# Kernel tuning notes

Hardware: AMD Instinct MI355X
Metric: run time of the kernel (lower is better)

The kernel has to match this reference:

```python
import jax, jax.numpy as jnp
import numpy as np

S, B, I, H, L = 256, 64, 512, 512, 2
EPS = 1e-5


def _layer_norm(x, g, b):
    m = jnp.mean(x, axis=-1, keepdims=True)
    v = jnp.var(x, axis=-1, keepdims=True)
    return (x - m) * jax.lax.rsqrt(v + EPS) * g + b


def setup_inputs() -> dict:
    key = jax.random.key(0)
    ks = jax.random.split(key, 8)
    gain = float(np.sqrt(1.0 / H))
    inputs = jax.random.normal(ks[0], (S, B, I), dtype=jnp.float32)
    h0 = jnp.zeros((L, B, H), dtype=jnp.float32)
    c0 = jnp.zeros((L, B, H), dtype=jnp.float32)
    # stacked weights (input_size == hidden_size so wx is uniform across layers)
    wx = jax.random.uniform(ks[1], (L, I, 4 * H), minval=-gain, maxval=gain, dtype=jnp.float32)
    wh = jax.random.uniform(ks[2], (L, H, 4 * H), minval=-gain, maxval=gain, dtype=jnp.float32)
    bias = jax.random.uniform(ks[3], (L, 4 * H), minval=-gain, maxval=gain, dtype=jnp.float32)
    # LayerNorm affine params: norm[2l] applied to x@wx, norm[2l+1] applied to h@wh
    ln_gx = jnp.ones((L, 4 * H), dtype=jnp.float32)
    ln_bx = jnp.zeros((L, 4 * H), dtype=jnp.float32)
    ln_gh = jnp.ones((L, 4 * H), dtype=jnp.float32)
    ln_bh = jnp.zeros((L, 4 * H), dtype=jnp.float32)
    return {"inputs": inputs, "h0": h0, "c0": c0, "wx": wx, "wh": wh,
            "bias": bias, "ln_gx": ln_gx, "ln_bx": ln_bx, "ln_gh": ln_gh, "ln_bh": ln_bh}


def reference(inputs, h0, c0, wx, wh, bias, ln_gx, ln_bx, ln_gh, ln_bh):
    x = inputs  # [S, B, I]
    hs, cs = [], []
    for l in range(L):
        # input-to-gate projection + its LayerNorm is time-independent: precompute
        xw = jnp.einsum('sbi,io->sbo', x, wx[l])            # [S, B, 4H]
        xn = _layer_norm(xw, ln_gx[l], ln_bx[l]) + bias[l]  # [S, B, 4H]
        whl, gh, bh = wh[l], ln_gh[l], ln_bh[l]

        def step(carry, xt):
            h, c = carry
            gate = xt + _layer_norm(h @ whl, gh, bh)        # [B, 4H]
            i, f, o, u = jnp.split(gate, 4, axis=-1)
            c = jax.nn.sigmoid(f) * c + jax.nn.sigmoid(i) * jnp.tanh(u)
            h = jax.nn.sigmoid(o) * jnp.tanh(c)
            return (h, c), h

        (hN, cN), ys = jax.lax.scan(step, (h0[l], c0[l]), xn)
        hs.append(hN)
        cs.append(cN)
        x = ys  # [S, B, H]
    h_n = jnp.stack(hs, axis=0)  # [L, B, H]
    c_n = jnp.stack(cs, axis=0)
    return x, h_n, c_n
```

## Files before the change

### kernel.cpp

```cpp
#include <hip/hip_runtime.h>

typedef unsigned short u16;
typedef _Float16 f16;
typedef __attribute__((ext_vector_type(8))) _Float16 f16x8;
typedef __attribute__((ext_vector_type(8))) unsigned short u16x8;
typedef __attribute__((ext_vector_type(4))) float f32x4;
typedef __attribute__((ext_vector_type(4))) unsigned u32x4;

#define NWG 32

__device__ __forceinline__ unsigned split2(float v) {
  f16 h = (f16)v;
  f16 l2 = (f16)((v - (float)h) * 2048.0f);
  return (unsigned)__builtin_bit_cast(u16, h) | ((unsigned)__builtin_bit_cast(u16, l2) << 16);
}

__global__ void k_zero(unsigned* __restrict__ part, unsigned* __restrict__ flg) {
  int i = blockIdx.x * blockDim.x + threadIdx.x;
  if (i < 8192) { part[i] = 0u; flg[i] = 0u; }
}

__global__ void k_wsplit(const float* __restrict__ wx, u16* __restrict__ th, u16* __restrict__ tl) {
  __shared__ float tile[32][33];
  int l = blockIdx.z;
  int n0 = blockIdx.x * 32, k0 = blockIdx.y * 32;
  int tx = threadIdx.x, ty = threadIdx.y;
  const float* src = wx + (size_t)l * 512 * 2048;
#pragma unroll
  for (int i = 0; i < 4; ++i)
    tile[ty + i * 8][tx] = src[(size_t)(k0 + ty + i * 8) * 2048 + n0 + tx];
  __syncthreads();
  u16* dh = th + (size_t)l * 2048 * 512;
  u16* dl = tl + (size_t)l * 2048 * 512;
#pragma unroll
  for (int i = 0; i < 4; ++i) {
    unsigned s = split2(tile[tx][ty + i * 8]);
    dh[(size_t)(n0 + ty + i * 8) * 512 + k0 + tx] = (u16)s;
    dl[(size_t)(n0 + ty + i * 8) * 512 + k0 + tx] = (u16)(s >> 16);
  }
}

__global__ void k_wlo(const float* __restrict__ wh, u16* __restrict__ wlo) {
  int idx = blockIdx.x * blockDim.x + threadIdx.x;
  int l = idx >> 17;
  int r = idx & 131071;
  int lane = r & 63;
  int fg = r >> 6;
  int kc = fg & 15, q = (fg >> 4) & 3, g = fg >> 6;
  int gcol = g * 16 + (lane & 15) + q * 512;
  int kb = kc * 32 + ((lane >> 4) << 3);
  const float* W = wh + (size_t)l * 512 * 2048;
  u16x8 o;
#pragma unroll
  for (int j = 0; j < 8; ++j)
    o[j] = (u16)(split2(W[(size_t)(kb + j) * 2048 + gcol]) >> 16);
  *(u16x8*)(wlo + (size_t)idx * 8) = o;
}

__global__ void __launch_bounds__(256, 1) k_gemm3(const float* __restrict__ A,
                                                  const u16* __restrict__ Bh, const u16* __restrict__ Bl,
                                                  float* __restrict__ C, int N, int K) {
  __shared__ u16 sA[2][128 * 64];
  __shared__ u16 sB[2][128 * 64];
  const int tid = threadIdx.x, l = tid & 63, w = tid >> 6;
  const int bx = blockIdx.x, by = blockIdx.y;
  const int wr = (w >> 1) * 64, wc = (w & 1) * 64;
  f32x4 acc0[4][4] = {}, acc1[4][4] = {};
  for (int k0 = 0; k0 < K; k0 += 64) {
#pragma unroll
    for (int s = 0; s < 4; ++s) {
      int cn = s * 256 + tid;
      int row = cn >> 3;
      int f0 = (cn & 7) * 8;
      int kb = f0 * 2;
      int sw = row * 128 + (kb ^ ((row & 7) << 4));
      const float* ap = A + ((size_t)(by * 128 + row) * K + k0 + f0);
      float4 a0 = *(const float4*)ap, a1 = *(const float4*)(ap + 4);
      float av[8] = {a0.x, a0.y, a0.z, a0.w, a1.x, a1.y, a1.z, a1.w};
      u16x8 ah_, al_;
#pragma unroll
      for (int j = 0; j < 8; ++j) {
        unsigned sp = split2(av[j]);
        ah_[j] = (u16)sp;
        al_[j] = (u16)(sp >> 16);
      }
      *(u16x8*)((char*)sA[0] + sw) = ah_;
      *(u16x8*)((char*)sA[1] + sw) = al_;
      size_t gb = (((size_t)(bx * 128 + row) * K + k0) << 1) + kb;
      *(u16x8*)((char*)sB[0] + sw) = *(const u16x8*)((const char*)Bh + gb);
      *(u16x8*)((char*)sB[1] + sw) = *(const u16x8*)((const char*)Bl + gb);
    }
    __syncthreads();
#pragma unroll
    for (int kc = 0; kc < 2; ++kc) {
      int kb = kc * 64 + (l >> 4) * 16;
      f16x8 ah[4], al[4], bh[4], bl[4];
#pragma unroll
      for (int mt = 0; mt < 4; ++mt) {
        int row = wr + mt * 16 + (l & 15);
        int off = row * 128 + (kb ^ ((row & 7) << 4));
        ah[mt] = *(const f16x8*)((const char*)sA[0] + off);
        al[mt] = *(const f16x8*)((const char*)sA[1] + off);
      }
#pragma unroll
      for (int nt = 0; nt < 4; ++nt) {
        int col = wc + nt * 16 + (l & 15);
        int off = col * 128 + (kb ^ ((col & 7) << 4));
        bh[nt] = *(const f16x8*)((const char*)sB[0] + off);
        bl[nt] = *(const f16x8*)((const char*)sB[1] + off);
      }
#pragma unroll
      for (int mt = 0; mt < 4; ++mt)
#pragma unroll
        for (int nt = 0; nt < 4; ++nt) {
          acc0[mt][nt] = __builtin_amdgcn_mfma_f32_16x16x32_f16(ah[mt], bh[nt], acc0[mt][nt], 0, 0, 0);
          acc1[mt][nt] = __builtin_amdgcn_mfma_f32_16x16x32_f16(ah[mt], bl[nt], acc1[mt][nt], 0, 0, 0);
          acc1[mt][nt] = __builtin_amdgcn_mfma_f32_16x16x32_f16(al[mt], bh[nt], acc1[mt][nt], 0, 0, 0);
        }
    }
    __syncthreads();
  }
#pragma unroll
  for (int mt = 0; mt < 4; ++mt)
#pragma unroll
    for (int nt = 0; nt < 4; ++nt)
#pragma unroll
      for (int j = 0; j < 4; ++j) {
        int row = by * 128 + wr + mt * 16 + ((l >> 4) << 2) + j;
        int col = bx * 128 + wc + nt * 16 + (l & 15);
        C[(size_t)row * N + col] = acc0[mt][nt][j] + acc1[mt][nt][j] * (1.0f / 2048.0f);
      }
}

__global__ void __launch_bounds__(256) k_ln2(float* __restrict__ X, const float* __restrict__ g,
                                             const float* __restrict__ b, const float* __restrict__ bias) {
  const int row = blockIdx.x, tid = threadIdx.x;
  float* rp = X + (size_t)row * 2048 + tid * 8;
  float4 v0 = *(const float4*)rp, v1 = *(const float4*)(rp + 4);
  float x[8] = {v0.x, v0.y, v0.z, v0.w, v1.x, v1.y, v1.z, v1.w};
  float s1 = 0.f, s2 = 0.f;
#pragma unroll
  for (int j = 0; j < 8; ++j) { s1 += x[j]; s2 += x[j] * x[j]; }
#pragma unroll
  for (int m = 1; m <= 32; m <<= 1) { s1 += __shfl_xor(s1, m, 64); s2 += __shfl_xor(s2, m, 64); }
  __shared__ float a1[4], a2[4];
  if ((tid & 63) == 0) { a1[tid >> 6] = s1; a2[tid >> 6] = s2; }
  __syncthreads();
  s1 = a1[0] + a1[1] + a1[2] + a1[3];
  s2 = a2[0] + a2[1] + a2[2] + a2[3];
  float mu = s1 * (1.f / 2048.f);
  float var = s2 * (1.f / 2048.f) - mu * mu;
  float rstd = 1.0f / sqrtf(var + 1e-5f);
#pragma unroll
  for (int j = 0; j < 8; ++j) {
    int c = tid * 8 + j;
    x[j] = (x[j] - mu) * rstd * g[c] + b[c] + bias[c];
  }
  *(float4*)rp = {x[0], x[1], x[2], x[3]};
  *(float4*)(rp + 4) = {x[4], x[5], x[6], x[7]};
}

__global__ void __launch_bounds__(256, 1) k_scan6(
    const float* __restrict__ wh, const u16* __restrict__ wlo,
    const float* __restrict__ gh, const float* __restrict__ bh,
    const float* __restrict__ xn, const float* __restrict__ h0l, const float* __restrict__ c0l,
    unsigned* __restrict__ hpubp, float* __restrict__ cspill,
    unsigned long long* __restrict__ part, unsigned* __restrict__ flags,
    float* __restrict__ ys, float* __restrict__ hn, float* __restrict__ cn,
    int t0, int first) {
  __shared__ u16 pk[32768];
  __shared__ u16 wl[32768];
  __shared__ float musd[128];
  const int tid = threadIdx.x;
  const int l = tid & 63, w = tid >> 6;
  const int g = blockIdx.x;
  const int lq = l >> 4, ll = l & 15;
  const int hcol = g * 16 + ll;

  const u16* wloG = wlo + (size_t)g * 32768;
  for (int c = tid; c < 4096; c += 256) {
    int lane = c & 63, kc = (c >> 6) & 15, q = c >> 10;
    int gcol = g * 16 + (lane & 15) + q * 512;
    int kb = kc * 32 + ((lane >> 4) << 3);
    u16x8 t8;
#pragma unroll
    for (int j = 0; j < 8; ++j)
      t8[j] = __builtin_bit_cast(u16, (f16)wh[(size_t)(kb + j) * 2048 + gcol]);
    *(u16x8*)(pk + (size_t)c * 8) = t8;
    *(u16x8*)(wl + (size_t)c * 8) = *(const u16x8*)(wloG + (size_t)c * 8);
  }
  float gam[4], bet[4];
#pragma unroll
  for (int q = 0; q < 4; ++q) { int gc = hcol + q * 512; gam[q] = gh[gc]; bet[q] = bh[gc]; }
  float cr[4];
#pragma unroll
  for (int j = 0; j < 4; ++j) {
    int r = w * 16 + lq * 4 + j;
    cr[j] = first ? c0l[r * 512 + hcol] : cspill[r * 512 + hcol];
  }
  if (first) {
    for (int u = tid; u < 1024; u += 256) {
      int row = 2 * g + (u >> 9), col = u & 511;
      __hip_atomic_store(&hpubp[row * 512 + col], split2(h0l[row * 512 + col]),
                         __ATOMIC_RELAXED, __HIP_MEMORY_SCOPE_AGENT);
    }
  }
  unsigned bid = 0;
#define BAR_ARRIVE()                                                                         \
  do {                                                                                       \
    bid++;                                                                                   \
    asm volatile("s_waitcnt vmcnt(0)" ::: "memory");                                         \
    __syncthreads();                                                                         \
    if (tid == 0)                                                                            \
      __hip_atomic_store(&flags[g * 32], bid, __ATOMIC_RELAXED, __HIP_MEMORY_SCOPE_AGENT);   \
  } while (0)
#define BAR_WAIT()                                                                           \
  do {                                                                                       \
    if (tid < NWG)                                                                           \
      while (__hip_atomic_load(&flags[tid * 32], __ATOMIC_RELAXED,                           \
                               __HIP_MEMORY_SCOPE_AGENT) < bid) {}                           \
    __builtin_amdgcn_fence(__ATOMIC_ACQUIRE, "agent");                                       \
  } while (0)

  float xp[16];
  BAR_ARRIVE();
#pragma unroll
  for (int q = 0; q < 4; ++q)
#pragma unroll
    for (int j = 0; j < 4; ++j)
      xp[q * 4 + j] = xn[(size_t)(w * 16 + lq * 4 + j) * 2048 + hcol + q * 512];
  BAR_WAIT();
  __syncthreads();

  for (int t = 0; t < 128; ++t) {
    const int p = (t0 + t) & 1;
    f32x4 acc0[4] = {}, acc1[4] = {};
#pragma unroll
    for (int kc = 0; kc < 16; ++kc) {
      const unsigned* hp = hpubp + ((size_t)(w * 16 + ll) * 512 + kc * 32 + lq * 8);
      uint4 pa = *(const uint4*)hp;
      uint4 pb = *(const uint4*)(hp + 4);
      u32x4 ahw, alw;
      ahw[0] = __builtin_amdgcn_perm(pa.y, pa.x, 0x05040100u);
      ahw[1] = __builtin_amdgcn_perm(pa.w, pa.z, 0x05040100u);
      ahw[2] = __builtin_amdgcn_perm(pb.y, pb.x, 0x05040100u);
      ahw[3] = __builtin_amdgcn_perm(pb.w, pb.z, 0x05040100u);
      alw[0] = __builtin_amdgcn_perm(pa.y, pa.x, 0x07060302u);
      alw[1] = __builtin_amdgcn_perm(pa.w, pa.z, 0x07060302u);
      alw[2] = __builtin_amdgcn_perm(pb.y, pb.x, 0x07060302u);
      alw[3] = __builtin_amdgcn_perm(pb.w, pb.z, 0x07060302u);
      f16x8 ah = __builtin_bit_cast(f16x8, ahw);
      f16x8 al = __builtin_bit_cast(f16x8, alw);
#pragma unroll
      for (int q = 0; q < 4; ++q) {
        f16x8 bhv = *(const f16x8*)(pk + ((size_t)(q * 16 + kc) * 64 + l) * 8);
        f16x8 blv = *(const f16x8*)(wl + ((size_t)(q * 16 + kc) * 64 + l) * 8);
        acc0[q] = __builtin_amdgcn_mfma_f32_16x16x32_f16(ah, bhv, acc0[q], 0, 0, 0);
        acc1[q] = __builtin_amdgcn_mfma_f32_16x16x32_f16(ah, blv, acc1[q], 0, 0, 0);
        acc1[q] = __builtin_amdgcn_mfma_f32_16x16x32_f16(al, bhv, acc1[q], 0, 0, 0);
      }
    }
    float y[4][4];
#pragma unroll
    for (int q = 0; q < 4; ++q)
#pragma unroll
      for (int j = 0; j < 4; ++j)
        y[q][j] = acc0[q][j] + acc1[q][j] * (1.0f / 2048.0f);

    float s1[4], s2[4];
#pragma unroll
    for (int j = 0; j < 4; ++j) {
      s1[j] = y[0][j] + y[1][j] + y[2][j] + y[3][j];
      s2[j] = y[0][j] * y[0][j] + y[1][j] * y[1][j] + y[2][j] * y[2][j] + y[3][j] * y[3][j];
    }
#pragma unroll
    for (int m = 1; m <= 8; m <<= 1)
#pragma unroll
      for (int j = 0; j < 4; ++j) {
        s1[j] += __shfl_xor(s1[j], m, 64);
        s2[j] += __shfl_xor(s2[j], m, 64);
      }
    if (ll == 0) {
#pragma unroll
      for (int j = 0; j < 4; ++j) {
        int r = w * 16 + lq * 4 + j;
        unsigned long long pv = ((unsigned long long)__builtin_bit_cast(unsigned, s2[j]) << 32) |
                                (unsigned long long)__builtin_bit_cast(unsigned, s1[j]);
        __hip_atomic_store(&part[(size_t)p * 2048 + (size_t)r * 32 + g], pv,
                           __ATOMIC_RELAXED, __HIP_MEMORY_SCOPE_AGENT);
      }
    }
    BAR_ARRIVE();
    BAR_WAIT();
    if (tid < 64) {
      const uint4* pp = (const uint4*)(part + (size_t)p * 2048 + (size_t)tid * 32);
      float a1 = 0.f, a2 = 0.f;
#pragma unroll
      for (int i = 0; i < 16; ++i) {
        uint4 v = pp[i];
        a1 += __builtin_bit_cast(float, v.x);
        a2 += __builtin_bit_cast(float, v.y);
        a1 += __builtin_bit_cast(float, v.z);
        a2 += __builtin_bit_cast(float, v.w);
      }
      float mu = a1 * (1.f / 2048.f);
      float ex2 = a2 * (1.f / 2048.f);
      musd[tid] = mu;
      musd[64 + tid] = 1.0f / sqrtf(ex2 - mu * mu + 1e-5f);
    }
    __syncthreads();
    float hs[4];
#pragma unroll
    for (int j = 0; j < 4; ++j) {
      int r = w * 16 + lq * 4 + j;
      float mu = musd[r], rstd = musd[64 + r];
      float gv[4];
#pragma unroll
      for (int q = 0; q < 4; ++q)
        gv[q] = (y[q][j] - mu) * rstd * gam[q] + bet[q] + xp[q * 4 + j];
      float fi = 1.f / (1.f + expf(-gv[0]));
      float ff = 1.f / (1.f + expf(-gv[1]));
      float fo = 1.f / (1.f + expf(-gv[2]));
      float fu = tanhf(gv[3]);
      cr[j] = ff * cr[j] + fi * fu;
      float h = fo * tanhf(cr[j]);
      hs[j] = h;
      __hip_atomic_store(&hpubp[(size_t)r * 512 + hcol], split2(h),
                         __ATOMIC_RELAXED, __HIP_MEMORY_SCOPE_AGENT);
    }
    BAR_ARRIVE();
#pragma unroll
    for (int j = 0; j < 4; ++j) {
      int r = w * 16 + lq * 4 + j;
      size_t ro = (size_t)r * 512 + hcol;
      __hip_atomic_store(&ys[(size_t)t * 32768 + ro], hs[j], __ATOMIC_RELAXED, __HIP_MEMORY_SCOPE_AGENT);
      if (t == 127)
        __hip_atomic_store(&cspill[ro], cr[j], __ATOMIC_RELAXED, __HIP_MEMORY_SCOPE_AGENT);
      if (t0 + t == 255) {
        __hip_atomic_store(&hn[ro], hs[j], __ATOMIC_RELAXED, __HIP_MEMORY_SCOPE_AGENT);
        __hip_atomic_store(&cn[ro], cr[j], __ATOMIC_RELAXED, __HIP_MEMORY_SCOPE_AGENT);
      }
    }
    if (t < 127) {
      const float* xrow = xn + (size_t)(t + 1) * 64 * 2048;
#pragma unroll
      for (int q = 0; q < 4; ++q)
#pragma unroll
        for (int j = 0; j < 4; ++j)
          xp[q * 4 + j] = xrow[(size_t)(w * 16 + lq * 4 + j) * 2048 + hcol + q * 512];
    }
    BAR_WAIT();
    __syncthreads();
  }
#undef BAR_ARRIVE
#undef BAR_WAIT
}

#define XN_OFF   0ull
#define WXH_OFF  67108864ull
#define WXL_OFF  71303168ull
#define WLO_OFF  75497472ull
#define HPP_OFF  79691776ull
#define CSP_OFF  79822848ull
#define PART_OFF 79953920ull
#define FLG_OFF  79986688ull

extern "C" void kernel_launch(void* const* d_in, const int* in_sizes, int n_in,
                              void* d_out, int out_size, void* d_ws, size_t ws_size,
                              hipStream_t stream) {
  const float* inputs = (const float*)d_in[0];
  const float* h0 = (const float*)d_in[1];
  const float* c0 = (const float*)d_in[2];
  const float* wx = (const float*)d_in[3];
  const float* wh = (const float*)d_in[4];
  const float* bias = (const float*)d_in[5];
  const float* gx = (const float*)d_in[6];
  const float* bxp = (const float*)d_in[7];
  const float* ghp = (const float*)d_in[8];
  const float* bhp = (const float*)d_in[9];
  float* out = (float*)d_out;
  char* ws = (char*)d_ws;

  float* xn = (float*)(ws + XN_OFF);
  u16* wxh = (u16*)(ws + WXH_OFF);
  u16* wxl = (u16*)(ws + WXL_OFF);
  u16* wlo = (u16*)(ws + WLO_OFF);
  unsigned* hpp = (unsigned*)(ws + HPP_OFF);
  float* csp = (float*)(ws + CSP_OFF);
  unsigned long long* part = (unsigned long long*)(ws + PART_OFF);
  unsigned* flg = (unsigned*)(ws + FLG_OFF);

  k_zero<<<32, 256, 0, stream>>>((unsigned*)(ws + PART_OFF), flg);
  k_wsplit<<<dim3(64, 16, 2), dim3(32, 8), 0, stream>>>(wx, wxh, wxl);
  k_wlo<<<1024, 256, 0, stream>>>(wh, wlo);

  for (int l = 0; l < 2; ++l) {
    const float* Abase = (l == 0) ? inputs : out;
    for (int k = 0; k < 2; ++k) {
      k_gemm3<<<dim3(16, 64), 256, 0, stream>>>(Abase + (size_t)k * 8192 * 512,
                                                wxh + (size_t)l * 2048 * 512,
                                                wxl + (size_t)l * 2048 * 512, xn, 2048, 512);
      k_ln2<<<8192, 256, 0, stream>>>(xn, gx + l * 2048, bxp + l * 2048, bias + l * 2048);
      k_scan6<<<NWG, 256, 0, stream>>>(wh + (size_t)l * 1048576, wlo + (size_t)l * 1048576,
                                       ghp + l * 2048, bhp + l * 2048, xn,
                                       h0 + (size_t)l * 32768, c0 + (size_t)l * 32768,
                                       hpp, csp, part, flg + (size_t)(l * 2 + k) * 2048,
                                       out + (size_t)k * 128 * 32768,
                                       out + 8388608 + (size_t)l * 32768,
                                       out + 8388608 + 65536 + (size_t)l * 32768,
                                       k * 128, (k == 0) ? 1 : 0);
    }
  }
}
```

Baseline: 7.080 ms.

## Run both LSTM layers concurrently in one wavefront-pipelined persistent scan kernel

Layer 1 no longer waits for all of layer 0. A single 64-workgroup persistent kernel runs layer 0 on half the workgroups and layer 1, one step behind, on the other half. Layer 1 computes its input projection and LayerNorm on the fly from layer 0's double-buffered published h. This drops the second input GEMM, the second LayerNorm pass and two scan launches. Weights are now pre-packed into MFMA fragment layout once, but layer 1 reads its low-part weight fragments from global memory each step, and cross-layer flag waits add synchronisation cost.

```diff
diff --git a/kernel.cpp b/kernel.cpp
--- a/kernel.cpp
+++ b/kernel.cpp
@@ -7,54 +7,51 @@
 typedef __attribute__((ext_vector_type(4))) float f32x4;
 typedef __attribute__((ext_vector_type(4))) unsigned u32x4;
 
-#define NWG 32
-
 __device__ __forceinline__ unsigned split2(float v) {
   f16 h = (f16)v;
   f16 l2 = (f16)((v - (float)h) * 2048.0f);
   return (unsigned)__builtin_bit_cast(u16, h) | ((unsigned)__builtin_bit_cast(u16, l2) << 16);
 }
 
-__global__ void k_zero(unsigned* __restrict__ part, unsigned* __restrict__ flg) {
+__device__ __forceinline__ unsigned fld(const unsigned* p) {
+  return __hip_atomic_load(p, __ATOMIC_RELAXED, __HIP_MEMORY_SCOPE_AGENT);
+}
+
+__global__ void k_zero(unsigned* __restrict__ z) {
   int i = blockIdx.x * blockDim.x + threadIdx.x;
-  if (i < 8192) { part[i] = 0u; flg[i] = 0u; }
+  if (i < 32768) z[i] = 0u;
 }
 
 __global__ void k_wsplit(const float* __restrict__ wx, u16* __restrict__ th, u16* __restrict__ tl) {
   __shared__ float tile[32][33];
-  int l = blockIdx.z;
   int n0 = blockIdx.x * 32, k0 = blockIdx.y * 32;
   int tx = threadIdx.x, ty = threadIdx.y;
-  const float* src = wx + (size_t)l * 512 * 2048;
 #pragma unroll
   for (int i = 0; i < 4; ++i)
-    tile[ty + i * 8][tx] = src[(size_t)(k0 + ty + i * 8) * 2048 + n0 + tx];
+    tile[ty + i * 8][tx] = wx[(size_t)(k0 + ty + i * 8) * 2048 + n0 + tx];
   __syncthreads();
-  u16* dh = th + (size_t)l * 2048 * 512;
-  u16* dl = tl + (size_t)l * 2048 * 512;
 #pragma unroll
   for (int i = 0; i < 4; ++i) {
     unsigned s = split2(tile[tx][ty + i * 8]);
-    dh[(size_t)(n0 + ty + i * 8) * 512 + k0 + tx] = (u16)s;
-    dl[(size_t)(n0 + ty + i * 8) * 512 + k0 + tx] = (u16)(s >> 16);
-  }
-}
-
-__global__ void k_wlo(const float* __restrict__ wh, u16* __restrict__ wlo) {
+    th[(size_t)(n0 + ty + i * 8) * 512 + k0 + tx] = (u16)s;
+    tl[(size_t)(n0 + ty + i * 8) * 512 + k0 + tx] = (u16)(s >> 16);
+  }
+}
+
+__global__ void k_pack(const float* __restrict__ W, u16* __restrict__ hi, u16* __restrict__ lo) {
   int idx = blockIdx.x * blockDim.x + threadIdx.x;
-  int l = idx >> 17;
-  int r = idx & 131071;
-  int lane = r & 63;
-  int fg = r >> 6;
-  int kc = fg & 15, q = (fg >> 4) & 3, g = fg >> 6;
+  int lane = idx & 63, kc = (idx >> 6) & 15, q = (idx >> 10) & 3, g = idx >> 12;
   int gcol = g * 16 + (lane & 15) + q * 512;
   int kb = kc * 32 + ((lane >> 4) << 3);
-  const float* W = wh + (size_t)l * 512 * 2048;
-  u16x8 o;
-#pragma unroll
-  for (int j = 0; j < 8; ++j)
-    o[j] = (u16)(split2(W[(size_t)(kb + j) * 2048 + gcol]) >> 16);
-  *(u16x8*)(wlo + (size_t)idx * 8) = o;
+  u16x8 oh, ol;
+#pragma unroll
+  for (int j = 0; j < 8; ++j) {
+    unsigned s = split2(W[(size_t)(kb + j) * 2048 + gcol]);
+    oh[j] = (u16)s;
+    ol[j] = (u16)(s >> 16);
+  }
+  *(u16x8*)(hi + (size_t)idx * 8) = oh;
+  *(u16x8*)(lo + (size_t)idx * 8) = ol;
 }
 
 __global__ void __launch_bounds__(256, 1) k_gemm3(const float* __restrict__ A,
@@ -160,48 +157,71 @@
   *(float4*)(rp + 4) = {x[4], x[5], x[6], x[7]};
 }
 
-__global__ void __launch_bounds__(256, 1) k_scan6(
-    const float* __restrict__ wh, const u16* __restrict__ wlo,
+__device__ __forceinline__ void unpk(uint4 a, uint4 b, f16x8& hi, f16x8& lo) {
+  u32x4 H, L;
+  H[0] = __builtin_amdgcn_perm(a.y, a.x, 0x05040100u);
+  H[1] = __builtin_amdgcn_perm(a.w, a.z, 0x05040100u);
+  H[2] = __builtin_amdgcn_perm(b.y, b.x, 0x05040100u);
+  H[3] = __builtin_amdgcn_perm(b.w, b.z, 0x05040100u);
+  L[0] = __builtin_amdgcn_perm(a.y, a.x, 0x07060302u);
+  L[1] = __builtin_amdgcn_perm(a.w, a.z, 0x07060302u);
+  L[2] = __builtin_amdgcn_perm(b.y, b.x, 0x07060302u);
+  L[3] = __builtin_amdgcn_perm(b.w, b.z, 0x07060302u);
+  hi = __builtin_bit_cast(f16x8, H);
+  lo = __builtin_bit_cast(f16x8, L);
+}
+
+__global__ void __launch_bounds__(256, 1) k_scan9(
+    const float* __restrict__ xn, const u16* __restrict__ frg,
+    const float* __restrict__ gx, const float* __restrict__ bx,
     const float* __restrict__ gh, const float* __restrict__ bh,
-    const float* __restrict__ xn, const float* __restrict__ h0l, const float* __restrict__ c0l,
-    unsigned* __restrict__ hpubp, float* __restrict__ cspill,
-    unsigned long long* __restrict__ part, unsigned* __restrict__ flags,
-    float* __restrict__ ys, float* __restrict__ hn, float* __restrict__ cn,
-    int t0, int first) {
+    const float* __restrict__ bias,
+    const float* __restrict__ h0, const float* __restrict__ c0,
+    unsigned* __restrict__ hp0, unsigned* __restrict__ hp1,
+    unsigned long long* __restrict__ pt0, unsigned long long* __restrict__ pt1,
+    unsigned* __restrict__ f0, unsigned* __restrict__ f1,
+    float* __restrict__ cs0, float* __restrict__ cs1,
+    float* __restrict__ out, int t0, int first) {
   __shared__ u16 pk[32768];
-  __shared__ u16 wl[32768];
-  __shared__ float musd[128];
+  __shared__ u16 sb[32768];
+  __shared__ float musd[256];
   const int tid = threadIdx.x;
   const int l = tid & 63, w = tid >> 6;
   const int g = blockIdx.x;
+  const int layer = g >> 5, gg = g & 31;
   const int lq = l >> 4, ll = l & 15;
-  const int hcol = g * 16 + ll;
-
-  const u16* wloG = wlo + (size_t)g * 32768;
+  const int hcol = gg * 16 + ll;
+  const bool L0 = (layer == 0);
+  unsigned* fown = L0 ? f0 : f1;
+  unsigned* foth = L0 ? f1 : f0;
+
+  const u16* pkG = frg + (size_t)(L0 ? 0 : 2) * 1048576 + (size_t)gg * 32768;
+  const u16* sbG = frg + (size_t)(L0 ? 1 : 4) * 1048576 + (size_t)gg * 32768;
+  const u16* whlG = frg + (size_t)3 * 1048576 + (size_t)gg * 32768;
+  const u16* wxlG = frg + (size_t)5 * 1048576 + (size_t)gg * 32768;
   for (int c = tid; c < 4096; c += 256) {
-    int lane = c & 63, kc = (c >> 6) & 15, q = c >> 10;
-    int gcol = g * 16 + (lane & 15) + q * 512;
-    int kb = kc * 32 + ((lane >> 4) << 3);
-    u16x8 t8;
-#pragma unroll
-    for (int j = 0; j < 8; ++j)
-      t8[j] = __builtin_bit_cast(u16, (f16)wh[(size_t)(kb + j) * 2048 + gcol]);
-    *(u16x8*)(pk + (size_t)c * 8) = t8;
-    *(u16x8*)(wl + (size_t)c * 8) = *(const u16x8*)(wloG + (size_t)c * 8);
-  }
-  float gam[4], bet[4];
-#pragma unroll
-  for (int q = 0; q < 4; ++q) { int gc = hcol + q * 512; gam[q] = gh[gc]; bet[q] = bh[gc]; }
+    *(u16x8*)(pk + (size_t)c * 8) = *(const u16x8*)(pkG + (size_t)c * 8);
+    *(u16x8*)(sb + (size_t)c * 8) = *(const u16x8*)(sbG + (size_t)c * 8);
+  }
+  float gxv[4], bxv[4], ghv[4], bhv[4], biv[4];
+#pragma unroll
+  for (int q = 0; q < 4; ++q) {
+    int gc = layer * 2048 + hcol + q * 512;
+    gxv[q] = gx[gc]; bxv[q] = bx[gc]; ghv[q] = gh[gc]; bhv[q] = bh[gc]; biv[q] = bias[gc];
+  }
   float cr[4];
-#pragma unroll
-  for (int j = 0; j < 4; ++j) {
-    int r = w * 16 + lq * 4 + j;
-    cr[j] = first ? c0l[r * 512 + hcol] : cspill[r * 512 + hcol];
+  {
+    const float* cl = first ? (c0 + (size_t)layer * 32768) : (L0 ? cs0 : cs1);
+#pragma unroll
+    for (int j = 0; j < 4; ++j)
+      cr[j] = cl[(w * 16 + lq * 4 + j) * 512 + hcol];
   }
   if (first) {
+    unsigned* dst = L0 ? (hp0 + 32768) : hp1;
     for (int u = tid; u < 1024; u += 256) {
-      int row = 2 * g + (u >> 9), col = u & 511;
-      __hip_atomic_store(&hpubp[row * 512 + col], split2(h0l[row * 512 + col]),
+      int row = 2 * gg + (u >> 9), col = u & 511;
+      __hip_atomic_store(&dst[row * 512 + col],
+                         split2(h0[(size_t)layer * 32768 + row * 512 + col]),
                          __ATOMIC_RELAXED, __HIP_MEMORY_SCOPE_AGENT);
     }
   }
@@ -212,158 +232,247 @@
     asm volatile("s_waitcnt vmcnt(0)" ::: "memory");                                         \
     __syncthreads();                                                                         \
     if (tid == 0)                                                                            \
-      __hip_atomic_store(&flags[g * 32], bid, __ATOMIC_RELAXED, __HIP_MEMORY_SCOPE_AGENT);   \
+      __hip_atomic_store(&fown[gg * 32], bid, __ATOMIC_RELAXED, __HIP_MEMORY_SCOPE_AGENT);   \
   } while (0)
-#define BAR_WAIT()                                                                           \
+#define BAR_WAIT(XEN, XTHR)                                                                  \
   do {                                                                                       \
-    if (tid < NWG)                                                                           \
-      while (__hip_atomic_load(&flags[tid * 32], __ATOMIC_RELAXED,                           \
-                               __HIP_MEMORY_SCOPE_AGENT) < bid) {}                           \
+    if (tid < 32) {                                                                          \
+      while (fld(&fown[tid * 32]) < bid) {}                                                  \
+    } else if (tid < 64 && (XEN)) {                                                          \
+      unsigned xt_ = (XTHR);                                                                 \
+      while (fld(&foth[(tid - 32) * 32]) < xt_) {}                                           \
+    }                                                                                        \
     __builtin_amdgcn_fence(__ATOMIC_ACQUIRE, "agent");                                       \
   } while (0)
 
   float xp[16];
   BAR_ARRIVE();
-#pragma unroll
-  for (int q = 0; q < 4; ++q)
-#pragma unroll
-    for (int j = 0; j < 4; ++j)
-      xp[q * 4 + j] = xn[(size_t)(w * 16 + lq * 4 + j) * 2048 + hcol + q * 512];
-  BAR_WAIT();
+  if (L0) {
+#pragma unroll
+    for (int q = 0; q < 4; ++q)
+#pragma unroll
+      for (int j = 0; j < 4; ++j)
+        xp[q * 4 + j] = xn[(size_t)(w * 16 + lq * 4 + j) * 2048 + hcol + q * 512];
+  }
+  BAR_WAIT(false, 0u);
   __syncthreads();
 
-  for (int t = 0; t < 128; ++t) {
-    const int p = (t0 + t) & 1;
-    f32x4 acc0[4] = {}, acc1[4] = {};
-#pragma unroll
-    for (int kc = 0; kc < 16; ++kc) {
-      const unsigned* hp = hpubp + ((size_t)(w * 16 + ll) * 512 + kc * 32 + lq * 8);
-      uint4 pa = *(const uint4*)hp;
-      uint4 pb = *(const uint4*)(hp + 4);
-      u32x4 ahw, alw;
-      ahw[0] = __builtin_amdgcn_perm(pa.y, pa.x, 0x05040100u);
-      ahw[1] = __builtin_amdgcn_perm(pa.w, pa.z, 0x05040100u);
-      ahw[2] = __builtin_amdgcn_perm(pb.y, pb.x, 0x05040100u);
-      ahw[3] = __builtin_amdgcn_perm(pb.w, pb.z, 0x05040100u);
-      alw[0] = __builtin_amdgcn_perm(pa.y, pa.x, 0x07060302u);
-      alw[1] = __builtin_amdgcn_perm(pa.w, pa.z, 0x07060302u);
-      alw[2] = __builtin_amdgcn_perm(pb.y, pb.x, 0x07060302u);
-      alw[3] = __builtin_amdgcn_perm(pb.w, pb.z, 0x07060302u);
-      f16x8 ah = __builtin_bit_cast(f16x8, ahw);
-      f16x8 al = __builtin_bit_cast(f16x8, alw);
-#pragma unroll
-      for (int q = 0; q < 4; ++q) {
-        f16x8 bhv = *(const f16x8*)(pk + ((size_t)(q * 16 + kc) * 64 + l) * 8);
-        f16x8 blv = *(const f16x8*)(wl + ((size_t)(q * 16 + kc) * 64 + l) * 8);
-        acc0[q] = __builtin_amdgcn_mfma_f32_16x16x32_f16(ah, bhv, acc0[q], 0, 0, 0);
-        acc1[q] = __builtin_amdgcn_mfma_f32_16x16x32_f16(ah, blv, acc1[q], 0, 0, 0);
-        acc1[q] = __builtin_amdgcn_mfma_f32_16x16x32_f16(al, bhv, acc1[q], 0, 0, 0);
-      }
-    }
-    float y[4][4];
-#pragma unroll
-    for (int q = 0; q < 4; ++q)
-#pragma unroll
-      for (int j = 0; j < 4; ++j)
-        y[q][j] = acc0[q][j] + acc1[q][j] * (1.0f / 2048.0f);
-
-    float s1[4], s2[4];
-#pragma unroll
-    for (int j = 0; j < 4; ++j) {
-      s1[j] = y[0][j] + y[1][j] + y[2][j] + y[3][j];
-      s2[j] = y[0][j] * y[0][j] + y[1][j] * y[1][j] + y[2][j] * y[2][j] + y[3][j] * y[3][j];
-    }
-#pragma unroll
-    for (int m = 1; m <= 8; m <<= 1)
+  for (int r = 0; r < 129; ++r) {
+    const bool act = L0 ? (r < 128) : (r >= 1);
+    const int tl = L0 ? r : r - 1;
+    const int t_abs = t0 + tl;
+    const int p = t_abs & 1;
+    float yx[4][4], yh[4][4];
+    if (act) {
+      if (L0) {
+        const unsigned* hb = hp0 + (size_t)(p ^ 1) * 32768;
+        f32x4 a0[4] = {}, a1[4] = {};
+#pragma unroll
+        for (int kc = 0; kc < 16; ++kc) {
+          const unsigned* hpx = hb + ((size_t)(w * 16 + ll) * 512 + kc * 32 + lq * 8);
+          f16x8 ah, al;
+          unpk(*(const uint4*)hpx, *(const uint4*)(hpx + 4), ah, al);
+#pragma unroll
+          for (int q = 0; q < 4; ++q) {
+            size_t fo = ((size_t)(q * 16 + kc) * 64 + l) * 8;
+            f16x8 bhv_ = *(const f16x8*)(pk + fo);
+            f16x8 blv_ = *(const f16x8*)(sb + fo);
+            a0[q] = __builtin_amdgcn_mfma_f32_16x16x32_f16(ah, bhv_, a0[q], 0, 0, 0);
+            a1[q] = __builtin_amdgcn_mfma_f32_16x16x32_f16(ah, blv_, a1[q], 0, 0, 0);
+            a1[q] = __builtin_amdgcn_mfma_f32_16x16x32_f16(al, bhv_, a1[q], 0, 0, 0);
+          }
+        }
+#pragma unroll
+        for (int q = 0; q < 4; ++q)
+#pragma unroll
+          for (int j = 0; j < 4; ++j)
+            yh[q][j] = a0[q][j] + a1[q][j] * (1.0f / 2048.0f);
+      } else {
+        const unsigned* xb = hp0 + (size_t)p * 32768;
+        f32x4 ax0[4] = {}, ax1[4] = {}, ah0[4] = {}, ah1[4] = {};
+#pragma unroll
+        for (int kc = 0; kc < 16; ++kc) {
+          size_t aoff = (size_t)(w * 16 + ll) * 512 + kc * 32 + lq * 8;
+          f16x8 xah, xal, hah, hal;
+          unpk(*(const uint4*)(xb + aoff), *(const uint4*)(xb + aoff + 4), xah, xal);
+          unpk(*(const uint4*)(hp1 + aoff), *(const uint4*)(hp1 + aoff + 4), hah, hal);
+#pragma unroll
+          for (int q = 0; q < 4; ++q) {
+            size_t fo = ((size_t)(q * 16 + kc) * 64 + l) * 8;
+            f16x8 whh_ = *(const f16x8*)(pk + fo);
+            f16x8 wxh_ = *(const f16x8*)(sb + fo);
+            f16x8 whl_ = *(const f16x8*)(whlG + fo);
+            f16x8 wxl_ = *(const f16x8*)(wxlG + fo);
+            ax0[q] = __builtin_amdgcn_mfma_f32_16x16x32_f16(xah, wxh_, ax0[q], 0, 0, 0);
+            ax1[q] = __builtin_amdgcn_mfma_f32_16x16x32_f16(xah, wxl_, ax1[q], 0, 0, 0);
+            ax1[q] = __builtin_amdgcn_mfma_f32_16x16x32_f16(xal, wxh_, ax1[q], 0, 0, 0);
+            ah0[q] = __builtin_amdgcn_mfma_f32_16x16x32_f16(hah, whh_, ah0[q], 0, 0, 0);
+            ah1[q] = __builtin_amdgcn_mfma_f32_16x16x32_f16(hah, whl_, ah1[q], 0, 0, 0);
+            ah1[q] = __builtin_amdgcn_mfma_f32_16x16x32_f16(hal, whh_, ah1[q], 0, 0, 0);
+          }
+        }
+#pragma unroll
+        for (int q = 0; q < 4; ++q)
+#pragma unroll
+          for (int j = 0; j < 4; ++j) {
+            yx[q][j] = ax0[q][j] + ax1[q][j] * (1.0f / 2048.0f);
+            yh[q][j] = ah0[q][j] + ah1[q][j] * (1.0f / 2048.0f);
+          }
+      }
+      float s1h[4], s2h[4], s1x[4], s2x[4];
 #pragma unroll
       for (int j = 0; j < 4; ++j) {
-        s1[j] += __shfl_xor(s1[j], m, 64);
-        s2[j] += __shfl_xor(s2[j], m, 64);
-      }
-    if (ll == 0) {
+        s1h[j] = yh[0][j] + yh[1][j] + yh[2][j] + yh[3][j];
+        s2h[j] = yh[0][j] * yh[0][j] + yh[1][j] * yh[1][j] + yh[2][j] * yh[2][j] + yh[3][j] * yh[3][j];
+        if (!L0) {
+          s1x[j] = yx[0][j] + yx[1][j] + yx[2][j] + yx[3][j];
+          s2x[j] = yx[0][j] * yx[0][j] + yx[1][j] * yx[1][j] + yx[2][j] * yx[2][j] + yx[3][j] * yx[3][j];
+        }
+      }
+#pragma unroll
+      for (int m = 1; m <= 8; m <<= 1)
+#pragma unroll
+        for (int j = 0; j < 4; ++j) {
+          s1h[j] += __shfl_xor(s1h[j], m, 64);
+          s2h[j] += __shfl_xor(s2h[j], m, 64);
+          if (!L0) {
+            s1x[j] += __shfl_xor(s1x[j], m, 64);
+            s2x[j] += __shfl_xor(s2x[j], m, 64);
+          }
+        }
+      if (ll == 0) {
+#pragma unroll
+        for (int j = 0; j < 4; ++j) {
+          int rr = w * 16 + lq * 4 + j;
+          unsigned long long vh = ((unsigned long long)__builtin_bit_cast(unsigned, s2h[j]) << 32) |
+                                  (unsigned long long)__builtin_bit_cast(unsigned, s1h[j]);
+          if (L0) {
+            __hip_atomic_store(&pt0[(size_t)p * 2048 + (size_t)rr * 32 + gg], vh,
+                               __ATOMIC_RELAXED, __HIP_MEMORY_SCOPE_AGENT);
+          } else {
+            unsigned long long vx = ((unsigned long long)__builtin_bit_cast(unsigned, s2x[j]) << 32) |
+                                    (unsigned long long)__builtin_bit_cast(unsigned, s1x[j]);
+            __hip_atomic_store(&pt1[((size_t)(p * 2 + 0) * 64 + rr) * 32 + gg], vx,
+                               __ATOMIC_RELAXED, __HIP_MEMORY_SCOPE_AGENT);
+            __hip_atomic_store(&pt1[((size_t)(p * 2 + 1) * 64 + rr) * 32 + gg], vh,
+                               __ATOMIC_RELAXED, __HIP_MEMORY_SCOPE_AGENT);
+          }
+        }
+      }
+    }
+    BAR_ARRIVE();
+    BAR_WAIT(L0 && r >= 2, bid - 2);
+    float hs[4];
+    if (act) {
+      if (tid < 64) {
+        if (L0) {
+          const uint4* pp = (const uint4*)(pt0 + (size_t)p * 2048 + (size_t)tid * 32);
+          float a1 = 0.f, a2 = 0.f;
+#pragma unroll
+          for (int i = 0; i < 16; ++i) {
+            uint4 v = pp[i];
+            a1 += __builtin_bit_cast(float, v.x); a2 += __builtin_bit_cast(float, v.y);
+            a1 += __builtin_bit_cast(float, v.z); a2 += __builtin_bit_cast(float, v.w);
+          }
+          float mu = a1 * (1.f / 2048.f), ex2 = a2 * (1.f / 2048.f);
+          musd[tid] = mu;
+          musd[64 + tid] = 1.0f / sqrtf(ex2 - mu * mu + 1e-5f);
+        } else {
+          const uint4* px = (const uint4*)(pt1 + ((size_t)(p * 2 + 0) * 64 + tid) * 32);
+          const uint4* ph = (const uint4*)(pt1 + ((size_t)(p * 2 + 1) * 64 + tid) * 32);
+          float a1x = 0.f, a2x = 0.f, a1h = 0.f, a2h = 0.f;
+#pragma unroll
+          for (int i = 0; i < 16; ++i) {
+            uint4 vx = px[i], vh = ph[i];
+            a1x += __builtin_bit_cast(float, vx.x); a2x += __builtin_bit_cast(float, vx.y);
+            a1x += __builtin_bit_cast(float, vx.z); a2x += __builtin_bit_cast(float, vx.w);
+            a1h += __builtin_bit_cast(float, vh.x); a2h += __builtin_bit_cast(float, vh.y);
+            a1h += __builtin_bit_cast(float, vh.z); a2h += __builtin_bit_cast(float, vh.w);
+          }
+          float mux = a1x * (1.f / 2048.f), ex2x = a2x * (1.f / 2048.f);
+          float muh = a1h * (1.f / 2048.f), ex2h = a2h * (1.f / 2048.f);
+          musd[tid] = mux;
+          musd[64 + tid] = 1.0f / sqrtf(ex2x - mux * mux + 1e-5f);
+          musd[128 + tid] = muh;
+          musd[192 + tid] = 1.0f / sqrtf(ex2h - muh * muh + 1e-5f);
+        }
+      }
+      __syncthreads();
 #pragma unroll
       for (int j = 0; j < 4; ++j) {
-        int r = w * 16 + lq * 4 + j;
-        unsigned long long pv = ((unsigned long long)__builtin_bit_cast(unsigned, s2[j]) << 32) |
-                                (unsigned long long)__builtin_bit_cast(unsigned, s1[j]);
-        __hip_atomic_store(&part[(size_t)p * 2048 + (size_t)r * 32 + g], pv,
-                           __ATOMIC_RELAXED, __HIP_MEMORY_SCOPE_AGENT);
+        int rr = w * 16 + lq * 4 + j;
+        float gv[4];
+        if (L0) {
+          float mu = musd[rr], rstd = musd[64 + rr];
+#pragma unroll
+          for (int q = 0; q < 4; ++q)
+            gv[q] = (yh[q][j] - mu) * rstd * ghv[q] + bhv[q] + xp[q * 4 + j];
+        } else {
+          float mux = musd[rr], rsx = musd[64 + rr];
+          float muh = musd[128 + rr], rsh = musd[192 + rr];
+#pragma unroll
+          for (int q = 0; q < 4; ++q)
+            gv[q] = (yx[q][j] - mux) * rsx * gxv[q] + bxv[q] + biv[q] +
+                    (yh[q][j] - muh) * rsh * ghv[q] + bhv[q];
+        }
+        float fi = 1.f / (1.f + expf(-gv[0]));
+        float ff = 1.f / (1.f + expf(-gv[1]));
+        float fo = 1.f / (1.f + expf(-gv[2]));
+        float fu = tanhf(gv[3]);
+        cr[j] = ff * cr[j] + fi * fu;
+        float h = fo * tanhf(cr[j]);
+        hs[j] = h;
+        size_t ro = (size_t)rr * 512 + hcol;
+        unsigned* dst = L0 ? (hp0 + (size_t)p * 32768) : hp1;
+        __hip_atomic_store(&dst[ro], split2(h), __ATOMIC_RELAXED, __HIP_MEMORY_SCOPE_AGENT);
       }
     }
     BAR_ARRIVE();
-    BAR_WAIT();
-    if (tid < 64) {
-      const uint4* pp = (const uint4*)(part + (size_t)p * 2048 + (size_t)tid * 32);
-      float a1 = 0.f, a2 = 0.f;
-#pragma unroll
-      for (int i = 0; i < 16; ++i) {
-        uint4 v = pp[i];
-        a1 += __builtin_bit_cast(float, v.x);
-        a2 += __builtin_bit_cast(float, v.y);
-        a1 += __builtin_bit_cast(float, v.z);
-        a2 += __builtin_bit_cast(float, v.w);
-      }
-      float mu = a1 * (1.f / 2048.f);
-      float ex2 = a2 * (1.f / 2048.f);
-      musd[tid] = mu;
-      musd[64 + tid] = 1.0f / sqrtf(ex2 - mu * mu + 1e-5f);
-    }
-    __syncthreads();
-    float hs[4];
-#pragma unroll
-    for (int j = 0; j < 4; ++j) {
-      int r = w * 16 + lq * 4 + j;
-      float mu = musd[r], rstd = musd[64 + r];
-      float gv[4];
-#pragma unroll
-      for (int q = 0; q < 4; ++q)
-        gv[q] = (y[q][j] - mu) * rstd * gam[q] + bet[q] + xp[q * 4 + j];
-      float fi = 1.f / (1.f + expf(-gv[0]));
-      float ff = 1.f / (1.f + expf(-gv[1]));
-      float fo = 1.f / (1.f + expf(-gv[2]));
-      float fu = tanhf(gv[3]);
-      cr[j] = ff * cr[j] + fi * fu;
-      float h = fo * tanhf(cr[j]);
-      hs[j] = h;
-      __hip_atomic_store(&hpubp[(size_t)r * 512 + hcol], split2(h),
-                         __ATOMIC_RELAXED, __HIP_MEMORY_SCOPE_AGENT);
-    }
-    BAR_ARRIVE();
-#pragma unroll
-    for (int j = 0; j < 4; ++j) {
-      int r = w * 16 + lq * 4 + j;
-      size_t ro = (size_t)r * 512 + hcol;
-      __hip_atomic_store(&ys[(size_t)t * 32768 + ro], hs[j], __ATOMIC_RELAXED, __HIP_MEMORY_SCOPE_AGENT);
-      if (t == 127)
-        __hip_atomic_store(&cspill[ro], cr[j], __ATOMIC_RELAXED, __HIP_MEMORY_SCOPE_AGENT);
-      if (t0 + t == 255) {
-        __hip_atomic_store(&hn[ro], hs[j], __ATOMIC_RELAXED, __HIP_MEMORY_SCOPE_AGENT);
-        __hip_atomic_store(&cn[ro], cr[j], __ATOMIC_RELAXED, __HIP_MEMORY_SCOPE_AGENT);
-      }
-    }
-    if (t < 127) {
-      const float* xrow = xn + (size_t)(t + 1) * 64 * 2048;
+    if (act) {
+#pragma unroll
+      for (int j = 0; j < 4; ++j) {
+        int rr = w * 16 + lq * 4 + j;
+        size_t ro = (size_t)rr * 512 + hcol;
+        if (!L0)
+          __hip_atomic_store(&out[(size_t)t_abs * 32768 + ro], hs[j],
+                             __ATOMIC_RELAXED, __HIP_MEMORY_SCOPE_AGENT);
+        if (tl == 127)
+          __hip_atomic_store(&(L0 ? cs0 : cs1)[ro], cr[j],
+                             __ATOMIC_RELAXED, __HIP_MEMORY_SCOPE_AGENT);
+        if (t_abs == 255) {
+          __hip_atomic_store(&out[8388608 + (size_t)layer * 32768 + ro], hs[j],
+                             __ATOMIC_RELAXED, __HIP_MEMORY_SCOPE_AGENT);
+          __hip_atomic_store(&out[8388608 + 65536 + (size_t)layer * 32768 + ro], cr[j],
+                             __ATOMIC_RELAXED, __HIP_MEMORY_SCOPE_AGENT);
+        }
+      }
+    }
+    if (L0 && r < 127) {
+      const float* xrow = xn + (size_t)(r + 1) * 64 * 2048;
 #pragma unroll
       for (int q = 0; q < 4; ++q)
 #pragma unroll
         for (int j = 0; j < 4; ++j)
           xp[q * 4 + j] = xrow[(size_t)(w * 16 + lq * 4 + j) * 2048 + hcol + q * 512];
     }
-    BAR_WAIT();
+    BAR_WAIT(!L0, bid);
     __syncthreads();
   }
 #undef BAR_ARRIVE
 #undef BAR_WAIT
 }
 
-#define XN_OFF   0ull
-#define WXH_OFF  67108864ull
-#define WXL_OFF  71303168ull
-#define WLO_OFF  75497472ull
-#define HPP_OFF  79691776ull
-#define CSP_OFF  79822848ull
-#define PART_OFF 79953920ull
-#define FLG_OFF  79986688ull
+#define XN_OFF  0ull
+#define WXH_OFF 67108864ull
+#define WXL_OFF 69206016ull
+#define FRG_OFF 71303168ull
+#define HP0_OFF 83886080ull
+#define HP1_OFF 84148224ull
+#define CS0_OFF 84279296ull
+#define CS1_OFF 84410368ull
+#define PT0_OFF 84541440ull
+#define PT1_OFF 84574208ull
+#define FLG_OFF 84639744ull
 
 extern "C" void kernel_launch(void* const* d_in, const int* in_sizes, int n_in,
                               void* d_out, int out_size, void* d_ws, size_t ws_size,
@@ -374,7 +483,7 @@
   const float* wx = (const float*)d_in[3];
   const float* wh = (const float*)d_in[4];
   const float* bias = (const float*)d_in[5];
-  const float* gx = (const float*)d_in[6];
+  const float* gxp = (const float*)d_in[6];
   const float* bxp = (const float*)d_in[7];
   const float* ghp = (const float*)d_in[8];
   const float* bhp = (const float*)d_in[9];
@@ -384,31 +493,29 @@
   float* xn = (float*)(ws + XN_OFF);
   u16* wxh = (u16*)(ws + WXH_OFF);
   u16* wxl = (u16*)(ws + WXL_OFF);
-  u16* wlo = (u16*)(ws + WLO_OFF);
-  unsigned* hpp = (unsigned*)(ws + HPP_OFF);
-  float* csp = (float*)(ws + CSP_OFF);
-  unsigned long long* part = (unsigned long long*)(ws + PART_OFF);
+  u16* frg = (u16*)(ws + FRG_OFF);
+  unsigned* hp0 = (unsigned*)(ws + HP0_OFF);
+  unsigned* hp1 = (unsigned*)(ws + HP1_OFF);
+  float* cs0 = (float*)(ws + CS0_OFF);
+  float* cs1 = (float*)(ws + CS1_OFF);
+  unsigned long long* pt0 = (unsigned long long*)(ws + PT0_OFF);
+  unsigned long long* pt1 = (unsigned long long*)(ws + PT1_OFF);
   unsigned* flg = (unsigned*)(ws + FLG_OFF);
 
-  k_zero<<<32, 256, 0, stream>>>((unsigned*)(ws + PART_OFF), flg);
-  k_wsplit<<<dim3(64, 16, 2), dim3(32, 8), 0, stream>>>(wx, wxh, wxl);
-  k_wlo<<<1024, 256, 0, stream>>>(wh, wlo);
-
-  for (int l = 0; l < 2; ++l) {
-    const float* Abase = (l == 0) ? inputs : out;
-    for (int k = 0; k < 2; ++k) {
-      k_gemm3<<<dim3(16, 64), 256, 0, stream>>>(Abase + (size_t)k * 8192 * 512,
-                                                wxh + (size_t)l * 2048 * 512,
-                                                wxl + (size_t)l * 2048 * 512, xn, 2048, 512);
-      k_ln2<<<8192, 256, 0, stream>>>(xn, gx + l * 2048, bxp + l * 2048, bias + l * 2048);
-      k_scan6<<<NWG, 256, 0, stream>>>(wh + (size_t)l * 1048576, wlo + (size_t)l * 1048576,
-                                       ghp + l * 2048, bhp + l * 2048, xn,
-                                       h0 + (size_t)l * 32768, c0 + (size_t)l * 32768,
-                                       hpp, csp, part, flg + (size_t)(l * 2 + k) * 2048,
-                                       out + (size_t)k * 128 * 32768,
-                                       out + 8388608 + (size_t)l * 32768,
-                                       out + 8388608 + 65536 + (size_t)l * 32768,
-                                       k * 128, (k == 0) ? 1 : 0);
-    }
-  }
-}
+  k_zero<<<128, 256, 0, stream>>>((unsigned*)(ws + PT0_OFF));
+  k_wsplit<<<dim3(64, 16), dim3(32, 8), 0, stream>>>(wx, wxh, wxl);
+  k_pack<<<512, 256, 0, stream>>>(wh, frg + (size_t)0 * 1048576, frg + (size_t)1 * 1048576);
+  k_pack<<<512, 256, 0, stream>>>(wh + 1048576, frg + (size_t)2 * 1048576, frg + (size_t)3 * 1048576);
+  k_pack<<<512, 256, 0, stream>>>(wx + 1048576, frg + (size_t)4 * 1048576, frg + (size_t)5 * 1048576);
+
+  for (int k = 0; k < 2; ++k) {
+    k_gemm3<<<dim3(16, 64), 256, 0, stream>>>(inputs + (size_t)k * 8192 * 512, wxh, wxl,
+                                              xn, 2048, 512);
+    k_ln2<<<8192, 256, 0, stream>>>(xn, gxp, bxp, bias);
+    k_scan9<<<64, 256, 0, stream>>>(xn, frg, gxp, bxp, ghp, bhp, bias, h0, c0,
+                                    hp0, hp1, pt0, pt1,
+                                    flg + (size_t)(k * 2 + 0) * 2048,
+                                    flg + (size_t)(k * 2 + 1) * 2048,
+                                    cs0, cs1, out, k * 128, (k == 0) ? 1 : 0);
+  }
+}
```

New measurement: 8.465 ms. +19.6%, slower.
